# Kernel tuning notes

Hardware: AMD Instinct MI355X
Metric: run time of the kernel (lower is better)

The kernel has to match this reference:

```python
import jax, jax.numpy as jnp
import numpy as np

# Mesh sizes: level-7 icosphere input, level-6 mesh for this Down block
VIN = 163842   # input vertices (level 7)
V = 40962      # nv_prev: vertices of down mesh (level 6)
F = 2 * V - 4  # 81920 faces
B, CIN, COUT = 4, 32, 64
DEG_L, DEG_G, DEG_F = 7, 3, 6  # nnz per row of L, G, F2V
EPS = 1e-5


def spmm(x, rows, cols, vals, nrows):
    """Sparse (nrows x K) @ dense x[B,C,K] -> [B,C,nrows] via gather + segment_sum."""
    g = x[..., cols] * vals                      # [B, C, nnz]
    b, c, nnz = g.shape
    out = jax.ops.segment_sum(g.reshape(b * c, nnz).T, rows,
                              num_segments=nrows, indices_are_sorted=True)
    return out.T.reshape(b, c, nrows)


def mesh_conv(x, coeffs, bias, Lrow, Lcol, Lval, Grow, Gcol, Gval,
              Frow, Fcol, Fval, EW, NS):
    # x: [B, C, V]
    identity = x
    lap = spmm(x, Lrow, Lcol, Lval, V)                       # [B,C,V]
    gf = spmm(x, Grow, Gcol, Gval, 3 * F)                    # [B,C,3F]
    b, c = x.shape[:2]
    gf = gf.reshape(b, c, 3, F).transpose(0, 1, 3, 2)        # [B,C,F,3]
    grad_ew = jnp.sum(gf * EW, axis=-1)                      # [B,C,F]
    grad_ns = jnp.sum(gf * NS, axis=-1)                      # [B,C,F]
    gv_ew = spmm(grad_ew, Frow, Fcol, Fval, V)               # [B,C,V]
    gv_ns = spmm(grad_ns, Frow, Fcol, Fval, V)               # [B,C,V]
    feat = jnp.stack([identity, lap, gv_ew, gv_ns], axis=-1)  # [B,C,V,4]
    return jnp.einsum('oik,bivk->bov', coeffs, feat) + bias[None, :, None]


def bn_relu(x, gamma, beta):
    # BatchNorm1d training mode: stats over (batch, vertex), biased variance
    mu = jnp.mean(x, axis=(0, 2), keepdims=True)
    var = jnp.var(x, axis=(0, 2), keepdims=True)
    xn = (x - mu) * jax.lax.rsqrt(var + EPS)
    return jax.nn.relu(xn * gamma[None, :, None] + beta[None, :, None])


def setup_inputs() -> dict:
    key = jax.random.key(0)
    ks = jax.random.split(key, 16)
    x = jax.random.normal(ks[0], (B, CIN, VIN), dtype=jnp.float32)
    # Sparse Laplacian L: V x V, 7 nnz per row (self + 6 neighbors)
    Lrow = jnp.repeat(jnp.arange(V, dtype=jnp.int32), DEG_L)
    Lcol = jax.random.randint(ks[1], (V * DEG_L,), 0, V, dtype=jnp.int32)
    Lval = jax.random.normal(ks[2], (V * DEG_L,), dtype=jnp.float32) * 0.1
    # Sparse gradient G: 3F x V, 3 nnz per row (face's 3 vertices)
    Grow = jnp.repeat(jnp.arange(3 * F, dtype=jnp.int32), DEG_G)
    Gcol = jax.random.randint(ks[3], (3 * F * DEG_G,), 0, V, dtype=jnp.int32)
    Gval = jax.random.normal(ks[4], (3 * F * DEG_G,), dtype=jnp.float32) * 0.1
    # Sparse face->vertex averaging F2V: V x F, 6 nnz per row
    Frow = jnp.repeat(jnp.arange(V, dtype=jnp.int32), DEG_F)
    Fcol = jax.random.randint(ks[5], (V * DEG_F,), 0, F, dtype=jnp.int32)
    Fval = jnp.full((V * DEG_F,), 1.0 / DEG_F, dtype=jnp.float32)
    # Face tangent basis vectors
    EW = jax.random.normal(ks[6], (F, 3), dtype=jnp.float32)
    NS = jax.random.normal(ks[7], (F, 3), dtype=jnp.float32)
    # Learned params: two MeshConv + two BatchNorm1d
    coeffs1 = jax.random.normal(ks[8], (COUT, CIN, 4), dtype=jnp.float32) * 0.1
    bias1 = jnp.zeros((COUT,), dtype=jnp.float32)
    gamma1 = jnp.ones((COUT,), dtype=jnp.float32)
    beta1 = jnp.zeros((COUT,), dtype=jnp.float32)
    coeffs2 = jax.random.normal(ks[9], (COUT, COUT, 4), dtype=jnp.float32) * 0.1
    bias2 = jnp.zeros((COUT,), dtype=jnp.float32)
    gamma2 = jnp.ones((COUT,), dtype=jnp.float32)
    beta2 = jnp.zeros((COUT,), dtype=jnp.float32)
    return dict(x=x, Lrow=Lrow, Lcol=Lcol, Lval=Lval, Grow=Grow, Gcol=Gcol,
                Gval=Gval, Frow=Frow, Fcol=Fcol, Fval=Fval, EW=EW, NS=NS,
                coeffs1=coeffs1, bias1=bias1, gamma1=gamma1, beta1=beta1,
                coeffs2=coeffs2, bias2=bias2, gamma2=gamma2, beta2=beta2)


def reference(x, Lrow, Lcol, Lval, Grow, Gcol, Gval, Frow, Fcol, Fval, EW, NS,
              coeffs1, bias1, gamma1, beta1, coeffs2, bias2, gamma2, beta2):
    # Down: restrict to coarser mesh vertices, then DoubleConv
    h = x[:, :, :V]
    h = mesh_conv(h, coeffs1, bias1, Lrow, Lcol, Lval, Grow, Gcol, Gval,
                  Frow, Fcol, Fval, EW, NS)
    h = bn_relu(h, gamma1, beta1)
    h = mesh_conv(h, coeffs2, bias2, Lrow, Lcol, Lval, Grow, Gcol, Gval,
                  Frow, Fcol, Fval, EW, NS)
    h = bn_relu(h, gamma2, beta2)
    return h
```

## Files before the change

kernel.cpp:

```cpp
#include <hip/hip_runtime.h>
#include <hip/hip_bf16.h>
#include <stdint.h>

#define NV    40962
#define NVIN  163842
#define NB    4
#define NCIN  32
#define NCOUT 64
#define NF    81920

typedef __attribute__((ext_vector_type(8))) short short8;
typedef __attribute__((ext_vector_type(4))) float f32x4;

static __device__ __forceinline__ uint32_t f2bf_rne(float f) {
  uint32_t u = __float_as_uint(f);
  return (u + 0x7fffu + ((u >> 16) & 1u)) >> 16;
}
static __device__ __forceinline__ float bf_lo(uint32_t u) { return __uint_as_float(u << 16); }
static __device__ __forceinline__ float bf_hi(uint32_t u) { return __uint_as_float(u & 0xffff0000u); }

__global__ __launch_bounds__(256) void k_transpose(const float* __restrict__ x,
                                                   uint32_t* __restrict__ xt32) {
  const int nvt = (NV + 63) >> 6;
  int bb = blockIdx.x / nvt;
  int v0 = (blockIdx.x % nvt) << 6;
  __shared__ float t[NCIN][65];
  int vi = threadIdx.x & 63, cg = threadIdx.x >> 6;
  int v = v0 + vi;
  for (int c = cg; c < NCIN; c += 4)
    t[c][vi] = (v < NV) ? x[(size_t)(bb * NCIN + c) * NVIN + v] : 0.f;
  __syncthreads();
  for (int i = threadIdx.x; i < 64 * 16; i += 256) {
    int v2 = i >> 4, cp = i & 15;
    int vv = v0 + v2;
    if (vv < NV)
      xt32[(size_t)vv * 64 + bb * 16 + cp] =
          (f2bf_rne(t[2 * cp + 1][v2]) << 16) | f2bf_rne(t[2 * cp][v2]);
  }
}

__global__ __launch_bounds__(256) void k_packB(const float* __restrict__ c1,
                                               const float* __restrict__ c2,
                                               uint4* __restrict__ pb1,
                                               uint4* __restrict__ pb2) {
  for (int u = threadIdx.x; u < 1024; u += 256) {
    int lane = u & 63, s = (u >> 6) % 4, nt = (u >> 6) / 4;
    int o = nt * 16 + (lane & 15);
    int kb = s * 32 + (lane >> 4) * 8;
    const float* cp = c1 + o * 128 + kb;
    uint4 wv;
    wv.x = (f2bf_rne(cp[1]) << 16) | f2bf_rne(cp[0]);
    wv.y = (f2bf_rne(cp[3]) << 16) | f2bf_rne(cp[2]);
    wv.z = (f2bf_rne(cp[5]) << 16) | f2bf_rne(cp[4]);
    wv.w = (f2bf_rne(cp[7]) << 16) | f2bf_rne(cp[6]);
    pb1[u] = wv;
  }
  for (int u = threadIdx.x; u < 2048; u += 256) {
    int lane = u & 63, s = (u >> 6) % 8, nt = (u >> 6) / 8;
    int o = nt * 16 + (lane & 15);
    int kb = s * 32 + (lane >> 4) * 8;
    const float* cp = c2 + o * 256 + kb;
    uint4 wv;
    wv.x = (f2bf_rne(cp[1]) << 16) | f2bf_rne(cp[0]);
    wv.y = (f2bf_rne(cp[3]) << 16) | f2bf_rne(cp[2]);
    wv.z = (f2bf_rne(cp[5]) << 16) | f2bf_rne(cp[4]);
    wv.w = (f2bf_rne(cp[7]) << 16) | f2bf_rne(cp[6]);
    pb2[u] = wv;
  }
}

template <int C>
__global__ __launch_bounds__(256) void k_grad(const uint32_t* __restrict__ xin32,
                                              const int* __restrict__ Gcol,
                                              const float* __restrict__ Gval,
                                              const float* __restrict__ EW,
                                              const float* __restrict__ NS,
                                              uint64_t* __restrict__ gg64) {
  constexpr int BC2 = NB * C / 2;
  constexpr int FP = 256 / BC2;
  const int p = threadIdx.x % BC2;
  const int fs = threadIdx.x / BC2;
  for (int f0 = blockIdx.x * FP; f0 < NF; f0 += gridDim.x * FP) {
    int f = __builtin_amdgcn_readfirstlane(f0 + fs);
    int gc[9]; float gv[9];
#pragma unroll
    for (int k = 0; k < 3; ++k) {
      int r = k * NF + f;
#pragma unroll
      for (int e = 0; e < 3; ++e) {
        gc[k * 3 + e] = Gcol[r * 3 + e];
        gv[k * 3 + e] = Gval[r * 3 + e];
      }
    }
    uint32_t xs[9];
#pragma unroll
    for (int i = 0; i < 9; ++i) xs[i] = xin32[(size_t)gc[i] * BC2 + p];
    float ew[3], ns[3];
#pragma unroll
    for (int k = 0; k < 3; ++k) { ew[k] = EW[f * 3 + k]; ns[k] = NS[f * 3 + k]; }
    float e0 = 0, e1 = 0, n0 = 0, n1 = 0;
#pragma unroll
    for (int k = 0; k < 3; ++k) {
      float g0 = gv[k * 3] * bf_lo(xs[k * 3]) + gv[k * 3 + 1] * bf_lo(xs[k * 3 + 1]) +
                 gv[k * 3 + 2] * bf_lo(xs[k * 3 + 2]);
      float g1 = gv[k * 3] * bf_hi(xs[k * 3]) + gv[k * 3 + 1] * bf_hi(xs[k * 3 + 1]) +
                 gv[k * 3 + 2] * bf_hi(xs[k * 3 + 2]);
      e0 += g0 * ew[k]; n0 += g0 * ns[k];
      e1 += g1 * ew[k]; n1 += g1 * ns[k];
    }
    uint32_t a = (f2bf_rne(n0) << 16) | f2bf_rne(e0);
    uint32_t b = (f2bf_rne(n1) << 16) | f2bf_rne(e1);
    gg64[(size_t)f * BC2 + p] = ((uint64_t)b << 32) | a;
  }
}

template <int C>
__global__ __launch_bounds__(256, 4) void k_conv_mfma(
    const uint32_t* __restrict__ xin32,
    const int* __restrict__ Lcol, const float* __restrict__ Lval,
    const int* __restrict__ Fcol, const float* __restrict__ Fval,
    const uint64_t* __restrict__ gg64,
    const uint4* __restrict__ pB,
    const float* __restrict__ bias,
    uint16_t* __restrict__ hout,
    float* __restrict__ bnS, float* __restrict__ bnQ) {
  constexpr int BC2 = NB * C / 2;
  constexpr int K = 4 * C;
  constexpr int K2 = 2 * K;
  constexpr int KS = K / 32;
  constexpr int VG = (C == 64) ? 8 : 16;
  constexpr int M = 4 * VG;
  constexpr int MT = M / 16;
  constexpr int WPM = 4 / MT;
  constexpr int NTC = MT;
  constexpr int VSTEP = 256 / BC2;

  __shared__ uint4 sA4[(M * K2) / 16];
  __shared__ float sS[64], sQ[64];
  if (threadIdx.x < 64) { sS[threadIdx.x] = 0.f; sQ[threadIdx.x] = 0.f; }

  const int tid = threadIdx.x;
  const int lane = tid & 63;
  const int w = tid >> 6;
  const int mtile = w / WPM;
  const int ntbase = (w % WPM) * NTC;
  const int col = lane & 15;
  const int lg = lane >> 4;

  const int p = tid % BC2;
  const int b = p / (C / 2);
  const int c0 = 2 * (p % (C / 2));
  const int vst = tid / BC2;

  float S[NTC], Q[NTC], bo[NTC];
#pragma unroll
  for (int t = 0; t < NTC; ++t) {
    S[t] = 0.f; Q[t] = 0.f;
    bo[t] = bias[(ntbase + t) * 16 + col];
  }
  __syncthreads();

  char* sA = (char*)sA4;
  const int npass = (NV + VG - 1) / VG;

  for (int it = blockIdx.x; it < npass; it += gridDim.x) {
    const int v0 = it * VG;
#pragma unroll
    for (int step = 0; step < VG / VSTEP; ++step) {
      int vl = step * VSTEP + vst;
      int v = v0 + vl;
      int m = vl * 4 + b;
      uint4 outv = {0u, 0u, 0u, 0u};
      if (v < NV) {
        int vu = __builtin_amdgcn_readfirstlane(v);
        uint32_t uid = xin32[(size_t)vu * BC2 + p];
        float l0 = 0.f, l1 = 0.f;
        {
          int lc[7]; float lw[7];
#pragma unroll
          for (int d = 0; d < 7; ++d) { lc[d] = Lcol[vu * 7 + d]; lw[d] = Lval[vu * 7 + d]; }
          uint32_t lx[7];
#pragma unroll
          for (int d = 0; d < 7; ++d) lx[d] = xin32[(size_t)lc[d] * BC2 + p];
#pragma unroll
          for (int d = 0; d < 7; ++d) { l0 += lw[d] * bf_lo(lx[d]); l1 += lw[d] * bf_hi(lx[d]); }
        }
        float e0 = 0, e1 = 0, n0 = 0, n1 = 0;
        {
          int fc[6]; float fw[6];
#pragma unroll
          for (int d = 0; d < 6; ++d) { fc[d] = Fcol[vu * 6 + d]; fw[d] = Fval[vu * 6 + d]; }
          uint64_t gx[6];
#pragma unroll
          for (int d = 0; d < 6; ++d) gx[d] = gg64[(size_t)fc[d] * BC2 + p];
#pragma unroll
          for (int d = 0; d < 6; ++d) {
            uint32_t ga = (uint32_t)gx[d], gb = (uint32_t)(gx[d] >> 32);
            e0 += fw[d] * bf_lo(ga); n0 += fw[d] * bf_hi(ga);
            e1 += fw[d] * bf_lo(gb); n1 += fw[d] * bf_hi(gb);
          }
        }
        outv.x = (f2bf_rne(l0) << 16) | (uid & 0xffffu);
        outv.y = (f2bf_rne(n0) << 16) | f2bf_rne(e0);
        outv.z = (f2bf_rne(l1) << 16) | (uid >> 16);
        outv.w = (f2bf_rne(n1) << 16) | f2bf_rne(e1);
      }
      int byteoff = m * K2 + ((c0 * 8) ^ ((m & 7) << 4));
      *(uint4*)(sA + byteoff) = outv;
    }
    __syncthreads();

    f32x4 acc[NTC];
#pragma unroll
    for (int t = 0; t < NTC; ++t) acc[t] = (f32x4){0.f, 0.f, 0.f, 0.f};
    const int marow = mtile * 16 + col;
    const int abase = marow * K2;
    const int aswz = (marow & 7) << 4;
#pragma unroll
    for (int s = 0; s < KS; ++s) {
      int kb = s * 32 + lg * 8;
      short8 af = *(const short8*)(sA + abase + ((kb * 2) ^ aswz));
#pragma unroll
      for (int t = 0; t < NTC; ++t) {
        short8 bf = *(const short8*)(pB + ((ntbase + t) * KS + s) * 64 + lane);
        acc[t] = __builtin_amdgcn_mfma_f32_16x16x32_bf16(af, bf, acc[t], 0, 0, 0);
      }
    }

#pragma unroll
    for (int t = 0; t < NTC; ++t) {
      int o = (ntbase + t) * 16 + col;
#pragma unroll
      for (int r = 0; r < 4; ++r) {
        int m = mtile * 16 + lg * 4 + r;
        int vl = m >> 2, b2 = m & 3;
        int v = v0 + vl;
        if (v < NV) {
          float h = acc[t][r] + bo[t];
          hout[((size_t)v * 4 + b2) * 64 + o] = (uint16_t)f2bf_rne(h);
          S[t] += h;
          Q[t] += h * h;
        }
      }
    }
    __syncthreads();
  }

#pragma unroll
  for (int t = 0; t < NTC; ++t) {
    int o = (ntbase + t) * 16 + col;
    atomicAdd(&sS[o], S[t]);
    atomicAdd(&sQ[o], Q[t]);
  }
  __syncthreads();
  if (threadIdx.x < 64) {
    atomicAdd(&bnS[threadIdx.x], sS[threadIdx.x]);
    atomicAdd(&bnQ[threadIdx.x], sQ[threadIdx.x]);
  }
}

__global__ void k_bnfin(const float* __restrict__ S, const float* __restrict__ Q,
                        const float* __restrict__ gamma, const float* __restrict__ beta,
                        float* __restrict__ scale, float* __restrict__ shift) {
  int o = threadIdx.x;
  if (o < NCOUT) {
    const float n = (float)((size_t)NB * NV);
    float mu = S[o] / n;
    float var = Q[o] / n - mu * mu;
    float sc = gamma[o] * rsqrtf(var + 1e-5f);
    scale[o] = sc;
    shift[o] = beta[o] - mu * sc;
  }
}

__global__ __launch_bounds__(256) void k_apply(uint32_t* __restrict__ h,
                                               const float* __restrict__ scale,
                                               const float* __restrict__ shift) {
  const int N = NV * 32;
  for (int i = blockIdx.x * 256 + threadIdx.x; i < N; i += gridDim.x * 256) {
    uint4 u = ((uint4*)h)[i];
    int o0 = (i * 8) & 63;
    uint32_t* uu = &u.x;
#pragma unroll
    for (int j = 0; j < 4; ++j) {
      float lo = fmaxf(0.f, bf_lo(uu[j]) * scale[o0 + 2 * j] + shift[o0 + 2 * j]);
      float hi = fmaxf(0.f, bf_hi(uu[j]) * scale[o0 + 2 * j + 1] + shift[o0 + 2 * j + 1]);
      uu[j] = (f2bf_rne(hi) << 16) | f2bf_rne(lo);
    }
    ((uint4*)h)[i] = u;
  }
}

__global__ __launch_bounds__(256) void k_final(const uint16_t* __restrict__ h2,
                                               const float* __restrict__ scale,
                                               const float* __restrict__ shift,
                                               float* __restrict__ out) {
  const int nvt = (NV + 63) >> 6;
  int b = blockIdx.x / nvt;
  int v0 = (blockIdx.x % nvt) << 6;
  __shared__ float t[64][65];
  int o = threadIdx.x & 63, vg = threadIdx.x >> 6;
  float sc = scale[o], sh = shift[o];
  for (int vi = vg; vi < 64; vi += 4) {
    int v = v0 + vi;
    float val = 0.f;
    if (v < NV) {
      uint32_t u = h2[(size_t)v * (NB * NCOUT) + b * NCOUT + o];
      val = __uint_as_float(u << 16);
    }
    t[o][vi] = fmaxf(0.f, val * sc + sh);
  }
  __syncthreads();
  int vi2 = threadIdx.x & 63, og = threadIdx.x >> 6;
  int v = v0 + vi2;
  for (int o2 = og; o2 < 64; o2 += 4) {
    if (v < NV) out[((size_t)b * NCOUT + o2) * NV + v] = t[o2][vi2];
  }
}

extern "C" void kernel_launch(void* const* d_in, const int* in_sizes, int n_in,
                              void* d_out, int out_size, void* d_ws, size_t ws_size,
                              hipStream_t stream) {
  const float* x       = (const float*)d_in[0];
  const int*   Lcol    = (const int*)d_in[2];
  const float* Lval    = (const float*)d_in[3];
  const int*   Gcol    = (const int*)d_in[5];
  const float* Gval    = (const float*)d_in[6];
  const int*   Fcol    = (const int*)d_in[8];
  const float* Fval    = (const float*)d_in[9];
  const float* EW      = (const float*)d_in[10];
  const float* NS      = (const float*)d_in[11];
  const float* coeffs1 = (const float*)d_in[12];
  const float* bias1   = (const float*)d_in[13];
  const float* gamma1  = (const float*)d_in[14];
  const float* beta1   = (const float*)d_in[15];
  const float* coeffs2 = (const float*)d_in[16];
  const float* bias2   = (const float*)d_in[17];
  const float* gamma2  = (const float*)d_in[18];
  const float* beta2   = (const float*)d_in[19];
  float* out           = (float*)d_out;

  uint32_t* xt = (uint32_t*)d_ws;
  uint64_t* gg = (uint64_t*)(xt + (size_t)NV * 64);
  uint32_t* h1 = (uint32_t*)(gg + (size_t)NF * 128);
  uint32_t* h2 = h1 + (size_t)NV * 128;
  float*    st = (float*)(h2 + (size_t)NV * 128);
  uint4*    pb1 = (uint4*)(st + 512);
  uint4*    pb2 = pb1 + 1024;
  float *S1 = st, *Q1 = st + 64, *S2 = st + 128, *Q2 = st + 192;
  float *sc1 = st + 256, *sh1 = st + 320, *sc2 = st + 384, *sh2 = st + 448;

  hipMemsetAsync(st, 0, 256 * sizeof(float), stream);

  const int nvt = (NV + 63) >> 6;
  k_packB<<<1, 256, 0, stream>>>(coeffs1, coeffs2, pb1, pb2);
  k_transpose<<<NB * nvt, 256, 0, stream>>>(x, xt);

  k_grad<NCIN><<<2048, 256, 0, stream>>>(xt, Gcol, Gval, EW, NS, gg);
  k_conv_mfma<NCIN><<<2048, 256, 0, stream>>>(xt, Lcol, Lval, Fcol, Fval, gg,
                                              pb1, bias1, (uint16_t*)h1, S1, Q1);
  k_bnfin<<<1, 64, 0, stream>>>(S1, Q1, gamma1, beta1, sc1, sh1);
  k_apply<<<2048, 256, 0, stream>>>(h1, sc1, sh1);

  k_grad<NCOUT><<<2048, 256, 0, stream>>>(h1, Gcol, Gval, EW, NS, gg);
  k_conv_mfma<NCOUT><<<2048, 256, 0, stream>>>(h1, Lcol, Lval, Fcol, Fval, gg,
                                               pb2, bias2, (uint16_t*)h2, S2, Q2);
  k_bnfin<<<1, 64, 0, stream>>>(S2, Q2, gamma2, beta2, sc2, sh2);
  k_final<<<NB * nvt, 256, 0, stream>>>((const uint16_t*)h2, sc2, sh2, out);
}
```

Before: 488.2 us.

## Fuse BN1+ReLU into second-layer gathers and widen per-thread channel loads

Removes the separate k_apply pass over h1 and instead applies the layer-1 batchnorm scale/shift and ReLU on the fly when k_grad and k_conv_mfma gather h1 values. For C=64, each thread now loads 4 channels (uint2/uint4) rather than 2, so the gathers are wider and fewer. The conv kernel is also changed from a grid-stride loop to one vertex group per block, with a grid sized to the vertex count. The trade is extra ALU work, since BN and ReLU are recomputed for every gathered neighbour, in exchange for saving a full read-write pass of h1 and a kernel launch.

```diff
diff --git a/kernel.cpp b/kernel.cpp
--- a/kernel.cpp
+++ b/kernel.cpp
@@ -18,6 +18,10 @@
 }
 static __device__ __forceinline__ float bf_lo(uint32_t u) { return __uint_as_float(u << 16); }
 static __device__ __forceinline__ float bf_hi(uint32_t u) { return __uint_as_float(u & 0xffff0000u); }
+
+static __device__ __forceinline__ void unp4(uint2 u, float* o) {
+  o[0] = bf_lo(u.x); o[1] = bf_hi(u.x); o[2] = bf_lo(u.y); o[3] = bf_hi(u.y);
+}
 
 __global__ __launch_bounds__(256) void k_transpose(const float* __restrict__ x,
                                                    uint32_t* __restrict__ xt32) {
@@ -69,52 +73,107 @@
   }
 }
 
-template <int C>
+template <int C, bool BN_IN>
 __global__ __launch_bounds__(256) void k_grad(const uint32_t* __restrict__ xin32,
                                               const int* __restrict__ Gcol,
                                               const float* __restrict__ Gval,
                                               const float* __restrict__ EW,
                                               const float* __restrict__ NS,
-                                              uint64_t* __restrict__ gg64) {
-  constexpr int BC2 = NB * C / 2;
-  constexpr int FP = 256 / BC2;
-  const int p = threadIdx.x % BC2;
-  const int fs = threadIdx.x / BC2;
-  for (int f0 = blockIdx.x * FP; f0 < NF; f0 += gridDim.x * FP) {
-    int f = __builtin_amdgcn_readfirstlane(f0 + fs);
-    int gc[9]; float gv[9];
-#pragma unroll
-    for (int k = 0; k < 3; ++k) {
-      int r = k * NF + f;
-#pragma unroll
-      for (int e = 0; e < 3; ++e) {
-        gc[k * 3 + e] = Gcol[r * 3 + e];
-        gv[k * 3 + e] = Gval[r * 3 + e];
-      }
-    }
-    uint32_t xs[9];
-#pragma unroll
-    for (int i = 0; i < 9; ++i) xs[i] = xin32[(size_t)gc[i] * BC2 + p];
-    float ew[3], ns[3];
-#pragma unroll
-    for (int k = 0; k < 3; ++k) { ew[k] = EW[f * 3 + k]; ns[k] = NS[f * 3 + k]; }
-    float e0 = 0, e1 = 0, n0 = 0, n1 = 0;
-#pragma unroll
-    for (int k = 0; k < 3; ++k) {
-      float g0 = gv[k * 3] * bf_lo(xs[k * 3]) + gv[k * 3 + 1] * bf_lo(xs[k * 3 + 1]) +
-                 gv[k * 3 + 2] * bf_lo(xs[k * 3 + 2]);
-      float g1 = gv[k * 3] * bf_hi(xs[k * 3]) + gv[k * 3 + 1] * bf_hi(xs[k * 3 + 1]) +
-                 gv[k * 3 + 2] * bf_hi(xs[k * 3 + 2]);
-      e0 += g0 * ew[k]; n0 += g0 * ns[k];
-      e1 += g1 * ew[k]; n1 += g1 * ns[k];
-    }
-    uint32_t a = (f2bf_rne(n0) << 16) | f2bf_rne(e0);
-    uint32_t b = (f2bf_rne(n1) << 16) | f2bf_rne(e1);
-    gg64[(size_t)f * BC2 + p] = ((uint64_t)b << 32) | a;
-  }
-}
-
-template <int C>
+                                              uint64_t* __restrict__ gg64,
+                                              const float* __restrict__ bnsc,
+                                              const float* __restrict__ bnsh) {
+  if constexpr (C == 64) {
+    const int p = threadIdx.x & 63;
+    const int fs = threadIdx.x >> 6;
+    float sc[4], sh[4];
+#pragma unroll
+    for (int j = 0; j < 4; ++j) {
+      sc[j] = BN_IN ? bnsc[4 * (p & 15) + j] : 1.f;
+      sh[j] = BN_IN ? bnsh[4 * (p & 15) + j] : 0.f;
+    }
+    const uint2* x2 = (const uint2*)xin32;
+    uint4* gg4 = (uint4*)gg64;
+    for (int f0 = blockIdx.x * 4; f0 < NF; f0 += gridDim.x * 4) {
+      int f = __builtin_amdgcn_readfirstlane(f0 + fs);
+      int gc[9]; float gv[9];
+#pragma unroll
+      for (int k = 0; k < 3; ++k) {
+        int r = k * NF + f;
+#pragma unroll
+        for (int e = 0; e < 3; ++e) {
+          gc[k * 3 + e] = Gcol[r * 3 + e];
+          gv[k * 3 + e] = Gval[r * 3 + e];
+        }
+      }
+      uint2 xs[9];
+#pragma unroll
+      for (int i = 0; i < 9; ++i) xs[i] = x2[(size_t)gc[i] * 64 + p];
+      float ew[3], ns[3];
+#pragma unroll
+      for (int k = 0; k < 3; ++k) { ew[k] = EW[f * 3 + k]; ns[k] = NS[f * 3 + k]; }
+      float e4[4] = {0, 0, 0, 0}, n4[4] = {0, 0, 0, 0};
+#pragma unroll
+      for (int k = 0; k < 3; ++k) {
+        float g[4] = {0, 0, 0, 0};
+#pragma unroll
+        for (int t = 0; t < 3; ++t) {
+          float v4[4];
+          unp4(xs[k * 3 + t], v4);
+#pragma unroll
+          for (int j = 0; j < 4; ++j) {
+            if (BN_IN) v4[j] = fmaxf(0.f, fmaf(v4[j], sc[j], sh[j]));
+            g[j] += gv[k * 3 + t] * v4[j];
+          }
+        }
+#pragma unroll
+        for (int j = 0; j < 4; ++j) { e4[j] += g[j] * ew[k]; n4[j] += g[j] * ns[k]; }
+      }
+      uint4 wv;
+      wv.x = (f2bf_rne(n4[0]) << 16) | f2bf_rne(e4[0]);
+      wv.y = (f2bf_rne(n4[1]) << 16) | f2bf_rne(e4[1]);
+      wv.z = (f2bf_rne(n4[2]) << 16) | f2bf_rne(e4[2]);
+      wv.w = (f2bf_rne(n4[3]) << 16) | f2bf_rne(e4[3]);
+      gg4[(size_t)f * 64 + p] = wv;
+    }
+  } else {
+    const int p = threadIdx.x & 63;
+    const int fs = threadIdx.x >> 6;
+    for (int f0 = blockIdx.x * 4; f0 < NF; f0 += gridDim.x * 4) {
+      int f = __builtin_amdgcn_readfirstlane(f0 + fs);
+      int gc[9]; float gv[9];
+#pragma unroll
+      for (int k = 0; k < 3; ++k) {
+        int r = k * NF + f;
+#pragma unroll
+        for (int e = 0; e < 3; ++e) {
+          gc[k * 3 + e] = Gcol[r * 3 + e];
+          gv[k * 3 + e] = Gval[r * 3 + e];
+        }
+      }
+      uint32_t xs[9];
+#pragma unroll
+      for (int i = 0; i < 9; ++i) xs[i] = xin32[(size_t)gc[i] * 64 + p];
+      float ew[3], ns[3];
+#pragma unroll
+      for (int k = 0; k < 3; ++k) { ew[k] = EW[f * 3 + k]; ns[k] = NS[f * 3 + k]; }
+      float e0 = 0, e1 = 0, n0 = 0, n1 = 0;
+#pragma unroll
+      for (int k = 0; k < 3; ++k) {
+        float g0 = gv[k * 3] * bf_lo(xs[k * 3]) + gv[k * 3 + 1] * bf_lo(xs[k * 3 + 1]) +
+                   gv[k * 3 + 2] * bf_lo(xs[k * 3 + 2]);
+        float g1 = gv[k * 3] * bf_hi(xs[k * 3]) + gv[k * 3 + 1] * bf_hi(xs[k * 3 + 1]) +
+                   gv[k * 3 + 2] * bf_hi(xs[k * 3 + 2]);
+        e0 += g0 * ew[k]; n0 += g0 * ns[k];
+        e1 += g1 * ew[k]; n1 += g1 * ns[k];
+      }
+      uint32_t a = (f2bf_rne(n0) << 16) | f2bf_rne(e0);
+      uint32_t b = (f2bf_rne(n1) << 16) | f2bf_rne(e1);
+      gg64[(size_t)f * 64 + p] = ((uint64_t)b << 32) | a;
+    }
+  }
+}
+
+template <int C, bool BN_IN>
 __global__ __launch_bounds__(256, 4) void k_conv_mfma(
     const uint32_t* __restrict__ xin32,
     const int* __restrict__ Lcol, const float* __restrict__ Lval,
@@ -122,9 +181,9 @@
     const uint64_t* __restrict__ gg64,
     const uint4* __restrict__ pB,
     const float* __restrict__ bias,
+    const float* __restrict__ bnsc, const float* __restrict__ bnsh,
     uint16_t* __restrict__ hout,
     float* __restrict__ bnS, float* __restrict__ bnQ) {
-  constexpr int BC2 = NB * C / 2;
   constexpr int K = 4 * C;
   constexpr int K2 = 2 * K;
   constexpr int KS = K / 32;
@@ -133,7 +192,6 @@
   constexpr int MT = M / 16;
   constexpr int WPM = 4 / MT;
   constexpr int NTC = MT;
-  constexpr int VSTEP = 256 / BC2;
 
   __shared__ uint4 sA4[(M * K2) / 16];
   __shared__ float sS[64], sQ[64];
@@ -147,11 +205,6 @@
   const int col = lane & 15;
   const int lg = lane >> 4;
 
-  const int p = tid % BC2;
-  const int b = p / (C / 2);
-  const int c0 = 2 * (p % (C / 2));
-  const int vst = tid / BC2;
-
   float S[NTC], Q[NTC], bo[NTC];
 #pragma unroll
   for (int t = 0; t < NTC; ++t) {
@@ -161,19 +214,98 @@
   __syncthreads();
 
   char* sA = (char*)sA4;
-  const int npass = (NV + VG - 1) / VG;
-
-  for (int it = blockIdx.x; it < npass; it += gridDim.x) {
-    const int v0 = it * VG;
-#pragma unroll
-    for (int step = 0; step < VG / VSTEP; ++step) {
-      int vl = step * VSTEP + vst;
+  const int v0 = blockIdx.x * VG;
+
+  if constexpr (C == 64) {
+    const int p = lane;
+    const int b = p >> 4;
+    const int c0q = p & 15;
+    float sc[4], sh[4];
+#pragma unroll
+    for (int j = 0; j < 4; ++j) {
+      sc[j] = BN_IN ? bnsc[4 * c0q + j] : 1.f;
+      sh[j] = BN_IN ? bnsh[4 * c0q + j] : 0.f;
+    }
+    const uint2* x2 = (const uint2*)xin32;
+    const uint4* gg4 = (const uint4*)gg64;
+#pragma unroll
+    for (int step = 0; step < 2; ++step) {
+      int vl = step * 4 + w;
       int v = v0 + vl;
       int m = vl * 4 + b;
-      uint4 outv = {0u, 0u, 0u, 0u};
+      uint4 o0 = {0, 0, 0, 0}, o1 = {0, 0, 0, 0};
       if (v < NV) {
         int vu = __builtin_amdgcn_readfirstlane(v);
-        uint32_t uid = xin32[(size_t)vu * BC2 + p];
+        float id4[4];
+        unp4(x2[(size_t)vu * 64 + p], id4);
+        float lap[4] = {0, 0, 0, 0};
+        {
+          int lc[7]; float lw[7];
+#pragma unroll
+          for (int d = 0; d < 7; ++d) { lc[d] = Lcol[vu * 7 + d]; lw[d] = Lval[vu * 7 + d]; }
+          uint2 lx[7];
+#pragma unroll
+          for (int d = 0; d < 7; ++d) lx[d] = x2[(size_t)lc[d] * 64 + p];
+#pragma unroll
+          for (int d = 0; d < 7; ++d) {
+            float v4[4];
+            unp4(lx[d], v4);
+#pragma unroll
+            for (int j = 0; j < 4; ++j) {
+              if (BN_IN) v4[j] = fmaxf(0.f, fmaf(v4[j], sc[j], sh[j]));
+              lap[j] += lw[d] * v4[j];
+            }
+          }
+        }
+        float e4[4] = {0, 0, 0, 0}, n4[4] = {0, 0, 0, 0};
+        {
+          int fc[6]; float fw[6];
+#pragma unroll
+          for (int d = 0; d < 6; ++d) { fc[d] = Fcol[vu * 6 + d]; fw[d] = Fval[vu * 6 + d]; }
+          uint4 gx[6];
+#pragma unroll
+          for (int d = 0; d < 6; ++d) gx[d] = gg4[(size_t)fc[d] * 64 + p];
+#pragma unroll
+          for (int d = 0; d < 6; ++d) {
+            const uint32_t* gu = &gx[d].x;
+#pragma unroll
+            for (int j = 0; j < 4; ++j) {
+              e4[j] += fw[d] * bf_lo(gu[j]);
+              n4[j] += fw[d] * bf_hi(gu[j]);
+            }
+          }
+        }
+        if (BN_IN) {
+#pragma unroll
+          for (int j = 0; j < 4; ++j) id4[j] = fmaxf(0.f, fmaf(id4[j], sc[j], sh[j]));
+        }
+        o0.x = (f2bf_rne(lap[0]) << 16) | f2bf_rne(id4[0]);
+        o0.y = (f2bf_rne(n4[0]) << 16) | f2bf_rne(e4[0]);
+        o0.z = (f2bf_rne(lap[1]) << 16) | f2bf_rne(id4[1]);
+        o0.w = (f2bf_rne(n4[1]) << 16) | f2bf_rne(e4[1]);
+        o1.x = (f2bf_rne(lap[2]) << 16) | f2bf_rne(id4[2]);
+        o1.y = (f2bf_rne(n4[2]) << 16) | f2bf_rne(e4[2]);
+        o1.z = (f2bf_rne(lap[3]) << 16) | f2bf_rne(id4[3]);
+        o1.w = (f2bf_rne(n4[3]) << 16) | f2bf_rne(e4[3]);
+      }
+      int base = m * K2;
+      int swz = (m & 7) << 4;
+      *(uint4*)(sA + base + ((c0q * 32) ^ swz)) = o0;
+      *(uint4*)(sA + base + ((c0q * 32 + 16) ^ swz)) = o1;
+    }
+  } else {
+    const int p = lane;
+    const int b = p >> 4;
+    const int c0 = 2 * (p & 15);
+#pragma unroll
+    for (int step = 0; step < 4; ++step) {
+      int vl = step * 4 + w;
+      int v = v0 + vl;
+      int m = vl * 4 + b;
+      uint4 outv = {0, 0, 0, 0};
+      if (v < NV) {
+        int vu = __builtin_amdgcn_readfirstlane(v);
+        uint32_t uid = xin32[(size_t)vu * 64 + p];
         float l0 = 0.f, l1 = 0.f;
         {
           int lc[7]; float lw[7];
@@ -181,7 +313,7 @@
           for (int d = 0; d < 7; ++d) { lc[d] = Lcol[vu * 7 + d]; lw[d] = Lval[vu * 7 + d]; }
           uint32_t lx[7];
 #pragma unroll
-          for (int d = 0; d < 7; ++d) lx[d] = xin32[(size_t)lc[d] * BC2 + p];
+          for (int d = 0; d < 7; ++d) lx[d] = xin32[(size_t)lc[d] * 64 + p];
 #pragma unroll
           for (int d = 0; d < 7; ++d) { l0 += lw[d] * bf_lo(lx[d]); l1 += lw[d] * bf_hi(lx[d]); }
         }
@@ -192,7 +324,7 @@
           for (int d = 0; d < 6; ++d) { fc[d] = Fcol[vu * 6 + d]; fw[d] = Fval[vu * 6 + d]; }
           uint64_t gx[6];
 #pragma unroll
-          for (int d = 0; d < 6; ++d) gx[d] = gg64[(size_t)fc[d] * BC2 + p];
+          for (int d = 0; d < 6; ++d) gx[d] = gg64[(size_t)fc[d] * 64 + p];
 #pragma unroll
           for (int d = 0; d < 6; ++d) {
             uint32_t ga = (uint32_t)gx[d], gb = (uint32_t)(gx[d] >> 32);
@@ -208,44 +340,43 @@
       int byteoff = m * K2 + ((c0 * 8) ^ ((m & 7) << 4));
       *(uint4*)(sA + byteoff) = outv;
     }
-    __syncthreads();
-
-    f32x4 acc[NTC];
-#pragma unroll
-    for (int t = 0; t < NTC; ++t) acc[t] = (f32x4){0.f, 0.f, 0.f, 0.f};
-    const int marow = mtile * 16 + col;
-    const int abase = marow * K2;
-    const int aswz = (marow & 7) << 4;
-#pragma unroll
-    for (int s = 0; s < KS; ++s) {
-      int kb = s * 32 + lg * 8;
-      short8 af = *(const short8*)(sA + abase + ((kb * 2) ^ aswz));
-#pragma unroll
-      for (int t = 0; t < NTC; ++t) {
-        short8 bf = *(const short8*)(pB + ((ntbase + t) * KS + s) * 64 + lane);
-        acc[t] = __builtin_amdgcn_mfma_f32_16x16x32_bf16(af, bf, acc[t], 0, 0, 0);
-      }
-    }
-
+  }
+  __syncthreads();
+
+  f32x4 acc[NTC];
+#pragma unroll
+  for (int t = 0; t < NTC; ++t) acc[t] = (f32x4){0.f, 0.f, 0.f, 0.f};
+  const int marow = mtile * 16 + col;
+  const int abase = marow * K2;
+  const int aswz = (marow & 7) << 4;
+#pragma unroll
+  for (int s = 0; s < KS; ++s) {
+    int kb = s * 32 + lg * 8;
+    short8 af = *(const short8*)(sA + abase + ((kb * 2) ^ aswz));
 #pragma unroll
     for (int t = 0; t < NTC; ++t) {
-      int o = (ntbase + t) * 16 + col;
-#pragma unroll
-      for (int r = 0; r < 4; ++r) {
-        int m = mtile * 16 + lg * 4 + r;
-        int vl = m >> 2, b2 = m & 3;
-        int v = v0 + vl;
-        if (v < NV) {
-          float h = acc[t][r] + bo[t];
-          hout[((size_t)v * 4 + b2) * 64 + o] = (uint16_t)f2bf_rne(h);
-          S[t] += h;
-          Q[t] += h * h;
-        }
-      }
-    }
-    __syncthreads();
-  }
-
+      short8 bf = *(const short8*)(pB + ((ntbase + t) * KS + s) * 64 + lane);
+      acc[t] = __builtin_amdgcn_mfma_f32_16x16x32_bf16(af, bf, acc[t], 0, 0, 0);
+    }
+  }
+
+#pragma unroll
+  for (int t = 0; t < NTC; ++t) {
+    int o = (ntbase + t) * 16 + col;
+#pragma unroll
+    for (int r = 0; r < 4; ++r) {
+      int m = mtile * 16 + lg * 4 + r;
+      int vl = m >> 2, b2 = m & 3;
+      int v = v0 + vl;
+      if (v < NV) {
+        float h = acc[t][r] + bo[t];
+        hout[((size_t)v * 4 + b2) * 64 + o] = (uint16_t)f2bf_rne(h);
+        S[t] += h;
+        Q[t] += h * h;
+      }
+    }
+  }
+  __syncthreads();
 #pragma unroll
   for (int t = 0; t < NTC; ++t) {
     int o = (ntbase + t) * 16 + col;
@@ -270,24 +401,6 @@
     float sc = gamma[o] * rsqrtf(var + 1e-5f);
     scale[o] = sc;
     shift[o] = beta[o] - mu * sc;
-  }
-}
-
-__global__ __launch_bounds__(256) void k_apply(uint32_t* __restrict__ h,
-                                               const float* __restrict__ scale,
-                                               const float* __restrict__ shift) {
-  const int N = NV * 32;
-  for (int i = blockIdx.x * 256 + threadIdx.x; i < N; i += gridDim.x * 256) {
-    uint4 u = ((uint4*)h)[i];
-    int o0 = (i * 8) & 63;
-    uint32_t* uu = &u.x;
-#pragma unroll
-    for (int j = 0; j < 4; ++j) {
-      float lo = fmaxf(0.f, bf_lo(uu[j]) * scale[o0 + 2 * j] + shift[o0 + 2 * j]);
-      float hi = fmaxf(0.f, bf_hi(uu[j]) * scale[o0 + 2 * j + 1] + shift[o0 + 2 * j + 1]);
-      uu[j] = (f2bf_rne(hi) << 16) | f2bf_rne(lo);
-    }
-    ((uint4*)h)[i] = u;
   }
 }
 
@@ -356,15 +469,18 @@
   k_packB<<<1, 256, 0, stream>>>(coeffs1, coeffs2, pb1, pb2);
   k_transpose<<<NB * nvt, 256, 0, stream>>>(x, xt);
 
-  k_grad<NCIN><<<2048, 256, 0, stream>>>(xt, Gcol, Gval, EW, NS, gg);
-  k_conv_mfma<NCIN><<<2048, 256, 0, stream>>>(xt, Lcol, Lval, Fcol, Fval, gg,
-                                              pb1, bias1, (uint16_t*)h1, S1, Q1);
+  k_grad<NCIN, false><<<2048, 256, 0, stream>>>(xt, Gcol, Gval, EW, NS, gg,
+                                                nullptr, nullptr);
+  k_conv_mfma<NCIN, false><<<(NV + 15) / 16, 256, 0, stream>>>(
+      xt, Lcol, Lval, Fcol, Fval, gg, pb1, bias1, nullptr, nullptr,
+      (uint16_t*)h1, S1, Q1);
   k_bnfin<<<1, 64, 0, stream>>>(S1, Q1, gamma1, beta1, sc1, sh1);
-  k_apply<<<2048, 256, 0, stream>>>(h1, sc1, sh1);
-
-  k_grad<NCOUT><<<2048, 256, 0, stream>>>(h1, Gcol, Gval, EW, NS, gg);
-  k_conv_mfma<NCOUT><<<2048, 256, 0, stream>>>(h1, Lcol, Lval, Fcol, Fval, gg,
-                                               pb2, bias2, (uint16_t*)h2, S2, Q2);
+
+  k_grad<NCOUT, true><<<2048, 256, 0, stream>>>(h1, Gcol, Gval, EW, NS, gg,
+                                                sc1, sh1);
+  k_conv_mfma<NCOUT, true><<<(NV + 7) / 8, 256, 0, stream>>>(
+      h1, Lcol, Lval, Fcol, Fval, gg, pb2, bias2, sc1, sh1,
+      (uint16_t*)h2, S2, Q2);
   k_bnfin<<<1, 64, 0, stream>>>(S2, Q2, gamma2, beta2, sc2, sh2);
   k_final<<<NB * nvt, 256, 0, stream>>>((const uint16_t*)h2, sc2, sh2, out);
 }
```

After: 547.0 us. 1.12x slower.
